# Performance work log

Measured on AMD Instinct MI355X. Metric: run time of the kernel, lower is better.

The kernel has to match this reference:

```python
import jax, jax.numpy as jnp
import numpy as np

N_NODES = 50000
ALPHA_SLOPE = 0.2  # LeakyReLU negative slope
EPS = 1e-16


def setup_inputs() -> dict:
    key = jax.random.key(0)
    k1, k2, k3, k4 = jax.random.split(key, 4)
    in_features, heads, d = 512, 8, 32
    x = jax.random.normal(k1, (N_NODES, in_features), dtype=jnp.float32)
    edge_index = jax.random.randint(k2, (2, 800000), 0, N_NODES, dtype=jnp.int64)
    # xavier_normal with relu gain ~ sqrt(2) * sqrt(2/(fan_in+fan_out))
    w_std = np.sqrt(2.0) * np.sqrt(2.0 / (in_features + d))
    a_std = np.sqrt(2.0) * np.sqrt(2.0 / (1 + 2 * d))
    W = jax.random.normal(k3, (heads, in_features, d), dtype=jnp.float32) * w_std
    a = jax.random.normal(k4, (heads, 2 * d), dtype=jnp.float32) * a_std
    return {"x": x, "edge_index": edge_index, "W": W, "a": a}


def reference(x, edge_index, W, a):
    # x: [N, F_in], edge_index: [2, E], W: [H, F_in, D], a: [H, 2D]
    n = x.shape[0]
    d = W.shape[-1]
    e0, e1 = edge_index[0], edge_index[1]
    # per-head projected features: [N, H, D]
    h = jnp.einsum('nf,hfd->nhd', x, W)
    # attention logits: a.mm(cat(h[e0], h[e1]).T) == a_src.h[e0] + a_dst.h[e1]
    a_src, a_dst = a[:, :d], a[:, d:]          # [H, D] each
    s_src = jnp.einsum('nhd,hd->nh', h, a_src)  # [N, H]
    s_dst = jnp.einsum('nhd,hd->nh', h, a_dst)  # [N, H]
    logits = s_src[e0] + s_dst[e1]              # [E, H]
    logits = jnp.where(logits >= 0, logits, ALPHA_SLOPE * logits)  # LeakyReLU
    # segment softmax over destination node e0
    m = jax.ops.segment_max(logits, e0, num_segments=n)   # [N, H]
    ex = jnp.exp(logits - m[e0])                          # [E, H]
    denom = jax.ops.segment_sum(ex, e0, num_segments=n)   # [N, H]
    alpha = ex / (denom[e0] + EPS)                        # [E, H]
    # dropout is identity in eval mode
    # sparse aggregate: out[e0] += alpha * h[e1]
    msg = alpha[:, :, None] * h[e1]                       # [E, H, D]
    out = jax.ops.segment_sum(msg, e0, num_segments=n)    # [N, H, D]
    return out.reshape(n, -1)                             # concat heads -> [N, H*D]
```

## Files before the change

### kernel.cpp

```cpp
#include <hip/hip_runtime.h>

#define N_NODES 50000
#define N_EDGES 800000
#define IN_F    512
#define HEADS   8
#define DHEAD   32
#define NHD     256
#define SLOPE   0.2f
#define EPS_F   1e-16f
#define N_SBLK  ((N_NODES + 255) / 256)
#define NB_GEMM ((N_NODES + 127) / 128)
#define NB_HIST ((N_EDGES + 4095) / 4096)

typedef __attribute__((ext_vector_type(8))) short short8;
typedef __attribute__((ext_vector_type(4))) float f32x4;
typedef __attribute__((ext_vector_type(4))) unsigned short u16x4;

__device__ __forceinline__ unsigned short f2bf(float f) {
  unsigned int u = __float_as_uint(f);
  unsigned int r = u + 0x7FFFu + ((u >> 16) & 1u);
  return (unsigned short)(r >> 16);
}
__device__ __forceinline__ float bf2f(unsigned short s) {
  return __uint_as_float(((unsigned int)s) << 16);
}
__device__ __forceinline__ void gload_lds16(const void* g, void* l) {
  __builtin_amdgcn_global_load_lds((const __attribute__((address_space(1))) void*)g,
                                   (__attribute__((address_space(3))) void*)l, 16, 0, 0);
}

__global__ void k_cast_w(const float* __restrict__ W, unsigned short* __restrict__ WbT,
                         int* __restrict__ deg) {
  int id = blockIdx.x * blockDim.x + threadIdx.x;
  if (id < NHD * IN_F) {
    int c = id >> 9, k = id & 511;
    WbT[id] = f2bf(W[(c >> 5) * (IN_F * DHEAD) + k * DHEAD + (c & 31)]);
  }
  if (id < N_NODES) deg[id] = 0;
}

__global__ __launch_bounds__(512) void k_gemm_mfma(const float* __restrict__ x,
                                                   const unsigned short* __restrict__ WbT,
                                                   unsigned short* __restrict__ hb,
                                                   const float* __restrict__ a,
                                                   float* __restrict__ s_src,
                                                   float* __restrict__ s_dst,
                                                   const int* __restrict__ ei,
                                                   int* __restrict__ deg) {
  if (blockIdx.x >= NB_GEMM) {
    int b = blockIdx.x - NB_GEMM;
    int end = min(b * 4096 + 4096, N_EDGES);
    for (int e = b * 4096 + threadIdx.x; e < end; e += 512)
      atomicAdd(&deg[ei[e]], 1);
    return;
  }

  __shared__ unsigned short As[128 * 64];
  __shared__ unsigned short Bs[256 * 64];
  const int tid  = threadIdx.x;
  const int lane = tid & 63;
  const int wid  = tid >> 6;
  const int wr   = wid >> 2;
  const int wc   = wid & 3;
  const int bm   = blockIdx.x * 128;

  const int ar0 = tid >> 3,          ap0 = tid & 7,          aq0 = ap0 ^ (ar0 & 7);
  const int ar1 = (tid + 512) >> 3,  ap1 = tid & 7,          aq1 = ap1 ^ (ar1 & 7);
  const float* gA0 = x + (size_t)min(bm + ar0, N_NODES - 1) * IN_F + aq0 * 8;
  const float* gA1 = x + (size_t)min(bm + ar1, N_NODES - 1) * IN_F + aq1 * 8;
  unsigned short* lA0 = &As[(ar0 * 8 + ap0) * 8];
  unsigned short* lA1 = &As[(ar1 * 8 + ap1) * 8];

  const int bs = 256 * wid + lane;
  const int brow = bs >> 3, bp = bs & 7, bq = bp ^ (brow & 7);
  const unsigned short* gB = WbT + (size_t)brow * IN_F + bq * 8;
  unsigned short* lB = &Bs[(size_t)bs * 8];

  f32x4 acc[4][4] = {};
  const int dl = lane & 15;
  const int qg = lane >> 4;

#pragma unroll
  for (int t = 0; t < 8; ++t) {
    const int k0 = t * 64;
    __syncthreads();
#pragma unroll
    for (int it = 0; it < 4; ++it)
      gload_lds16(gB + k0 + (size_t)it * 8 * IN_F, lB + it * 64 * 8);
    {
      float4 a00 = *(const float4*)(gA0 + k0);
      float4 a01 = *(const float4*)(gA0 + k0 + 4);
      float4 a10 = *(const float4*)(gA1 + k0);
      float4 a11 = *(const float4*)(gA1 + k0 + 4);
      short8 v0, v1;
      v0[0] = (short)f2bf(a00.x); v0[1] = (short)f2bf(a00.y);
      v0[2] = (short)f2bf(a00.z); v0[3] = (short)f2bf(a00.w);
      v0[4] = (short)f2bf(a01.x); v0[5] = (short)f2bf(a01.y);
      v0[6] = (short)f2bf(a01.z); v0[7] = (short)f2bf(a01.w);
      v1[0] = (short)f2bf(a10.x); v1[1] = (short)f2bf(a10.y);
      v1[2] = (short)f2bf(a10.z); v1[3] = (short)f2bf(a10.w);
      v1[4] = (short)f2bf(a11.x); v1[5] = (short)f2bf(a11.y);
      v1[6] = (short)f2bf(a11.z); v1[7] = (short)f2bf(a11.w);
      *(short8*)lA0 = v0;
      *(short8*)lA1 = v1;
    }
    __syncthreads();

#pragma unroll
    for (int kk = 0; kk < 2; ++kk) {
      const int kq = kk * 4 + qg;
      short8 af[4], bfr[4];
#pragma unroll
      for (int i = 0; i < 4; ++i) {
        int r = wr * 64 + i * 16 + dl;
        af[i] = *(const short8*)&As[(r * 8 + (kq ^ (r & 7))) * 8];
      }
#pragma unroll
      for (int j = 0; j < 4; ++j) {
        int c = wc * 64 + j * 16 + dl;
        bfr[j] = *(const short8*)&Bs[(c * 8 + (kq ^ (c & 7))) * 8];
      }
#pragma unroll
      for (int i = 0; i < 4; ++i)
#pragma unroll
        for (int j = 0; j < 4; ++j)
          acc[i][j] = __builtin_amdgcn_mfma_f32_16x16x32_bf16(af[i], bfr[j], acc[i][j], 0, 0, 0);
    }
  }

  const int h0 = 2 * wc, h1 = 2 * wc + 1;
  const int cb = wc * 64;
  const float as00 = a[h0 * 64 + dl],      as01 = a[h0 * 64 + 16 + dl];
  const float as10 = a[h1 * 64 + dl],      as11 = a[h1 * 64 + 16 + dl];
  const float ad00 = a[h0 * 64 + 32 + dl], ad01 = a[h0 * 64 + 48 + dl];
  const float ad10 = a[h1 * 64 + 32 + dl], ad11 = a[h1 * 64 + 48 + dl];

#pragma unroll
  for (int i = 0; i < 4; ++i) {
#pragma unroll
    for (int q = 0; q < 4; ++q) {
      int row = bm + wr * 64 + i * 16 + qg * 4 + q;
      float ss0 = acc[i][0][q] * as00 + acc[i][1][q] * as01;
      float ss1 = acc[i][2][q] * as10 + acc[i][3][q] * as11;
      float sd0 = acc[i][0][q] * ad00 + acc[i][1][q] * ad01;
      float sd1 = acc[i][2][q] * ad10 + acc[i][3][q] * ad11;
#pragma unroll
      for (int o = 1; o < 16; o <<= 1) {
        ss0 += __shfl_xor(ss0, o);
        ss1 += __shfl_xor(ss1, o);
        sd0 += __shfl_xor(sd0, o);
        sd1 += __shfl_xor(sd1, o);
      }
      if (row < N_NODES) {
#pragma unroll
        for (int j = 0; j < 4; ++j)
          hb[(size_t)row * NHD + cb + j * 16 + dl] = f2bf(acc[i][j][q]);
        if (dl == 0) {
          s_src[row * 8 + h0] = ss0;
          s_src[row * 8 + h1] = ss1;
          s_dst[row * 8 + h0] = sd0;
          s_dst[row * 8 + h1] = sd1;
        }
      }
    }
  }
}

__global__ __launch_bounds__(256) void k_bsum(const int* __restrict__ deg,
                                              int* __restrict__ bsum) {
  __shared__ int sm[4];
  int i = blockIdx.x * 256 + threadIdx.x;
  int v = (i < N_NODES) ? deg[i] : 0;
#pragma unroll
  for (int o = 1; o < 64; o <<= 1) v += __shfl_xor(v, o);
  if ((threadIdx.x & 63) == 0) sm[threadIdx.x >> 6] = v;
  __syncthreads();
  if (threadIdx.x == 0) bsum[blockIdx.x] = sm[0] + sm[1] + sm[2] + sm[3];
}

__global__ __launch_bounds__(256) void k_scan_main(const int* __restrict__ deg,
                                                   const int* __restrict__ bsum,
                                                   int* __restrict__ rowptr,
                                                   int* __restrict__ cursor) {
  __shared__ int sb[256];
  __shared__ int sm[256];
  const int t = threadIdx.x;
  const int b = blockIdx.x;
  int bv = (t < N_SBLK) ? bsum[t] : 0;
  sb[t] = bv;
  int i = b * 256 + t;
  int v = (i < N_NODES) ? deg[i] : 0;
  sm[t] = v;
  __syncthreads();
#pragma unroll
  for (int o = 1; o < 256; o <<= 1) {
    int u1 = (t >= o) ? sb[t - o] : 0;
    int u2 = (t >= o) ? sm[t - o] : 0;
    __syncthreads();
    sb[t] += u1;
    sm[t] += u2;
    __syncthreads();
  }
  int boff = (b > 0) ? sb[b - 1] : 0;
  if (i < N_NODES) {
    int ex = boff + sm[t] - v;
    rowptr[i] = ex;
    cursor[i] = ex;
  }
  if (b == 0 && t == 0) rowptr[N_NODES] = sb[255];
}

__global__ void k_fill(const int* __restrict__ ei, int* __restrict__ cursor,
                       int* __restrict__ edst) {
  int e = blockIdx.x * blockDim.x + threadIdx.x;
  if (e >= N_EDGES) return;
  int p = atomicAdd(&cursor[ei[e]], 1);
  edst[p] = ei[N_EDGES + e];
}

__global__ __launch_bounds__(256) void k_aggr(const int* __restrict__ rowptr,
                                              const int* __restrict__ edst,
                                              const float* __restrict__ s_src,
                                              const float* __restrict__ s_dst,
                                              const unsigned short* __restrict__ hb,
                                              float* __restrict__ out) {
  int n = (int)((blockIdx.x * blockDim.x + threadIdx.x) >> 6);
  if (n >= N_NODES) return;
  n = __builtin_amdgcn_readfirstlane(n);
  const int lane = threadIdx.x & 63;
  const int head = lane >> 3;
  const float ssrc = s_src[n * 8 + head];
  int i = rowptr[n];
  const int iend = rowptr[n + 1];
  float den = 0.f;
  f32x4 acc = {0.f, 0.f, 0.f, 0.f};
  for (; i + 1 < iend; i += 2) {
    int d0 = edst[i], d1 = edst[i + 1];
    float v0 = ssrc + s_dst[d0 * 8 + head];
    float v1 = ssrc + s_dst[d1 * 8 + head];
    u16x4 h0 = *(const u16x4*)(hb + (size_t)d0 * NHD + lane * 4);
    u16x4 h1 = *(const u16x4*)(hb + (size_t)d1 * NHD + lane * 4);
    v0 = v0 >= 0.f ? v0 : SLOPE * v0;
    v1 = v1 >= 0.f ? v1 : SLOPE * v1;
    float e0 = __expf(v0), e1 = __expf(v1);
    den += e0 + e1;
    acc.x += e0 * bf2f(h0.x) + e1 * bf2f(h1.x);
    acc.y += e0 * bf2f(h0.y) + e1 * bf2f(h1.y);
    acc.z += e0 * bf2f(h0.z) + e1 * bf2f(h1.z);
    acc.w += e0 * bf2f(h0.w) + e1 * bf2f(h1.w);
  }
  if (i < iend) {
    int d0 = edst[i];
    float v0 = ssrc + s_dst[d0 * 8 + head];
    v0 = v0 >= 0.f ? v0 : SLOPE * v0;
    float e0 = __expf(v0);
    u16x4 h0 = *(const u16x4*)(hb + (size_t)d0 * NHD + lane * 4);
    den += e0;
    acc.x += e0 * bf2f(h0.x);
    acc.y += e0 * bf2f(h0.y);
    acc.z += e0 * bf2f(h0.z);
    acc.w += e0 * bf2f(h0.w);
  }
  float inv = 1.f / (den + EPS_F);
  *(f32x4*)(out + (size_t)n * NHD + lane * 4) = acc * inv;
}

extern "C" void kernel_launch(void* const* d_in, const int* in_sizes, int n_in,
                              void* d_out, int out_size, void* d_ws, size_t ws_size,
                              hipStream_t stream) {
  const float* x  = (const float*)d_in[0];
  const int*   ei = (const int*)d_in[1];
  const float* W  = (const float*)d_in[2];
  const float* a  = (const float*)d_in[3];
  float* out = (float*)d_out;

  unsigned short* hb  = (unsigned short*)d_ws;
  unsigned short* WbT = hb + (size_t)N_NODES * NHD;
  float* s_src = (float*)(WbT + (size_t)NHD * IN_F);
  float* s_dst = s_src + (size_t)N_NODES * HEADS;
  int* deg    = (int*)(s_dst + (size_t)N_NODES * HEADS);
  int* cursor = deg + N_NODES;
  int* rowptr = cursor + N_NODES;
  int* bsum   = rowptr + 50008;
  int* edst   = bsum + 256;

  k_cast_w<<<512, 256, 0, stream>>>(W, WbT, deg);
  k_gemm_mfma<<<NB_GEMM + NB_HIST, 512, 0, stream>>>(x, WbT, hb, a, s_src, s_dst, ei, deg);
  k_bsum<<<N_SBLK, 256, 0, stream>>>(deg, bsum);
  k_scan_main<<<N_SBLK, 256, 0, stream>>>(deg, bsum, rowptr, cursor);
  k_fill<<<(N_EDGES + 255) / 256, 256, 0, stream>>>(ei, cursor, edst);
  k_aggr<<<(N_NODES * 64 + 255) / 256, 256, 0, stream>>>(rowptr, edst, s_src, s_dst, hb, out);
}
```

Before: 175.2 us.

## Overlap CSR edge fill with GEMM blocks and move histogram into prep kernel

Result: slower. 183.3 us (+4.6%).

```diff
diff --git a/kernel.cpp b/kernel.cpp
--- a/kernel.cpp
+++ b/kernel.cpp
@@ -11,6 +11,7 @@
 #define N_SBLK  ((N_NODES + 255) / 256)
 #define NB_GEMM ((N_NODES + 127) / 128)
 #define NB_HIST ((N_EDGES + 4095) / 4096)
+#define NB_MIX  (NB_GEMM * 5)
 
 typedef __attribute__((ext_vector_type(8))) short short8;
 typedef __attribute__((ext_vector_type(4))) float f32x4;
@@ -29,14 +30,67 @@
                                    (__attribute__((address_space(3))) void*)l, 16, 0, 0);
 }
 
-__global__ void k_cast_w(const float* __restrict__ W, unsigned short* __restrict__ WbT,
-                         int* __restrict__ deg) {
-  int id = blockIdx.x * blockDim.x + threadIdx.x;
-  if (id < NHD * IN_F) {
-    int c = id >> 9, k = id & 511;
-    WbT[id] = f2bf(W[(c >> 5) * (IN_F * DHEAD) + k * DHEAD + (c & 31)]);
-  }
-  if (id < N_NODES) deg[id] = 0;
+__global__ __launch_bounds__(256) void k_prep(const float* __restrict__ W,
+                                              unsigned short* __restrict__ WbT,
+                                              const int* __restrict__ ei,
+                                              int* __restrict__ deg) {
+  int b = blockIdx.x;
+  if (b < 512) {
+    int id = b * 256 + threadIdx.x;
+    if (id < NHD * IN_F) {
+      int c = id >> 9, k = id & 511;
+      WbT[id] = f2bf(W[(c >> 5) * (IN_F * DHEAD) + k * DHEAD + (c & 31)]);
+    }
+  } else {
+    int hb_ = b - 512;
+    int end = min(hb_ * 4096 + 4096, N_EDGES);
+    for (int e = hb_ * 4096 + threadIdx.x; e < end; e += 256)
+      atomicAdd(&deg[ei[e]], 1);
+  }
+}
+
+__global__ __launch_bounds__(256) void k_bsum(const int* __restrict__ deg,
+                                              int* __restrict__ bsum) {
+  __shared__ int sm[4];
+  int i = blockIdx.x * 256 + threadIdx.x;
+  int v = (i < N_NODES) ? deg[i] : 0;
+#pragma unroll
+  for (int o = 1; o < 64; o <<= 1) v += __shfl_xor(v, o);
+  if ((threadIdx.x & 63) == 0) sm[threadIdx.x >> 6] = v;
+  __syncthreads();
+  if (threadIdx.x == 0) bsum[blockIdx.x] = sm[0] + sm[1] + sm[2] + sm[3];
+}
+
+__global__ __launch_bounds__(256) void k_scan_main(const int* __restrict__ deg,
+                                                   const int* __restrict__ bsum,
+                                                   int* __restrict__ rowptr,
+                                                   int* __restrict__ cursor) {
+  __shared__ int sb[256];
+  __shared__ int sm[256];
+  const int t = threadIdx.x;
+  const int b = blockIdx.x;
+  int bv = (t < N_SBLK) ? bsum[t] : 0;
+  sb[t] = bv;
+  int i = b * 256 + t;
+  int v = (i < N_NODES) ? deg[i] : 0;
+  sm[t] = v;
+  __syncthreads();
+#pragma unroll
+  for (int o = 1; o < 256; o <<= 1) {
+    int u1 = (t >= o) ? sb[t - o] : 0;
+    int u2 = (t >= o) ? sm[t - o] : 0;
+    __syncthreads();
+    sb[t] += u1;
+    sm[t] += u2;
+    __syncthreads();
+  }
+  int boff = (b > 0) ? sb[b - 1] : 0;
+  if (i < N_NODES) {
+    int ex = boff + sm[t] - v;
+    rowptr[i] = ex;
+    cursor[i] = ex;
+  }
+  if (b == 0 && t == 0) rowptr[N_NODES] = sb[255];
 }
 
 __global__ __launch_bounds__(512) void k_gemm_mfma(const float* __restrict__ x,
@@ -46,12 +100,16 @@
                                                    float* __restrict__ s_src,
                                                    float* __restrict__ s_dst,
                                                    const int* __restrict__ ei,
-                                                   int* __restrict__ deg) {
-  if (blockIdx.x >= NB_GEMM) {
-    int b = blockIdx.x - NB_GEMM;
-    int end = min(b * 4096 + 4096, N_EDGES);
-    for (int e = b * 4096 + threadIdx.x; e < end; e += 512)
-      atomicAdd(&deg[ei[e]], 1);
+                                                   int* __restrict__ cursor,
+                                                   int* __restrict__ edst) {
+  const int bid = blockIdx.x;
+  if ((bid % 5) != 4) {
+    int fid = (bid / 5) * 4 + (bid % 5);
+    int e = fid * 512 + threadIdx.x;
+    if (e < N_EDGES) {
+      int p = atomicAdd(&cursor[ei[e]], 1);
+      edst[p] = ei[N_EDGES + e];
+    }
     return;
   }
 
@@ -62,7 +120,7 @@
   const int wid  = tid >> 6;
   const int wr   = wid >> 2;
   const int wc   = wid & 3;
-  const int bm   = blockIdx.x * 128;
+  const int bm   = (bid / 5) * 128;
 
   const int ar0 = tid >> 3,          ap0 = tid & 7,          aq0 = ap0 ^ (ar0 & 7);
   const int ar1 = (tid + 512) >> 3,  ap1 = tid & 7,          aq1 = ap1 ^ (ar1 & 7);
@@ -164,58 +222,6 @@
       }
     }
   }
-}
-
-__global__ __launch_bounds__(256) void k_bsum(const int* __restrict__ deg,
-                                              int* __restrict__ bsum) {
-  __shared__ int sm[4];
-  int i = blockIdx.x * 256 + threadIdx.x;
-  int v = (i < N_NODES) ? deg[i] : 0;
-#pragma unroll
-  for (int o = 1; o < 64; o <<= 1) v += __shfl_xor(v, o);
-  if ((threadIdx.x & 63) == 0) sm[threadIdx.x >> 6] = v;
-  __syncthreads();
-  if (threadIdx.x == 0) bsum[blockIdx.x] = sm[0] + sm[1] + sm[2] + sm[3];
-}
-
-__global__ __launch_bounds__(256) void k_scan_main(const int* __restrict__ deg,
-                                                   const int* __restrict__ bsum,
-                                                   int* __restrict__ rowptr,
-                                                   int* __restrict__ cursor) {
-  __shared__ int sb[256];
-  __shared__ int sm[256];
-  const int t = threadIdx.x;
-  const int b = blockIdx.x;
-  int bv = (t < N_SBLK) ? bsum[t] : 0;
-  sb[t] = bv;
-  int i = b * 256 + t;
-  int v = (i < N_NODES) ? deg[i] : 0;
-  sm[t] = v;
-  __syncthreads();
-#pragma unroll
-  for (int o = 1; o < 256; o <<= 1) {
-    int u1 = (t >= o) ? sb[t - o] : 0;
-    int u2 = (t >= o) ? sm[t - o] : 0;
-    __syncthreads();
-    sb[t] += u1;
-    sm[t] += u2;
-    __syncthreads();
-  }
-  int boff = (b > 0) ? sb[b - 1] : 0;
-  if (i < N_NODES) {
-    int ex = boff + sm[t] - v;
-    rowptr[i] = ex;
-    cursor[i] = ex;
-  }
-  if (b == 0 && t == 0) rowptr[N_NODES] = sb[255];
-}
-
-__global__ void k_fill(const int* __restrict__ ei, int* __restrict__ cursor,
-                       int* __restrict__ edst) {
-  int e = blockIdx.x * blockDim.x + threadIdx.x;
-  if (e >= N_EDGES) return;
-  int p = atomicAdd(&cursor[ei[e]], 1);
-  edst[p] = ei[N_EDGES + e];
 }
 
 __global__ __launch_bounds__(256) void k_aggr(const int* __restrict__ rowptr,
@@ -284,10 +290,10 @@
   int* bsum   = rowptr + 50008;
   int* edst   = bsum + 256;
 
-  k_cast_w<<<512, 256, 0, stream>>>(W, WbT, deg);
-  k_gemm_mfma<<<NB_GEMM + NB_HIST, 512, 0, stream>>>(x, WbT, hb, a, s_src, s_dst, ei, deg);
+  hipMemsetAsync(deg, 0, (size_t)N_NODES * sizeof(int), stream);
+  k_prep<<<512 + NB_HIST, 256, 0, stream>>>(W, WbT, ei, deg);
   k_bsum<<<N_SBLK, 256, 0, stream>>>(deg, bsum);
   k_scan_main<<<N_SBLK, 256, 0, stream>>>(deg, bsum, rowptr, cursor);
-  k_fill<<<(N_EDGES + 255) / 256, 256, 0, stream>>>(ei, cursor, edst);
+  k_gemm_mfma<<<NB_MIX, 512, 0, stream>>>(x, WbT, hb, a, s_src, s_dst, ei, cursor, edst);
   k_aggr<<<(N_NODES * 64 + 255) / 256, 256, 0, stream>>>(rowptr, edst, s_src, s_dst, hb, out);
 }
```
